# Kernel optimization log

Hardware: AMD Instinct MI355X
Metric: run time of the kernel (lower is better)

The kernel has to match this reference:

```python
import jax, jax.numpy as jnp
import numpy as np

B, T, C, H = 2, 2048, 1024, 16
D = C // H  # head dim = 64


def setup_inputs() -> dict:
    key = jax.random.key(0)
    ks = jax.random.split(key, 9)
    x = jax.random.normal(ks[0], (B, T, C), dtype=jnp.float32)
    # causal mask: True above the diagonal => positions to mask out
    mask = jnp.triu(jnp.ones((T, T), dtype=bool), k=1)[None, None]  # [1,1,T,T]
    s = 0.02
    Wq = jax.random.normal(ks[1], (C, C), dtype=jnp.float32) * s
    Wk = jax.random.normal(ks[2], (C, C), dtype=jnp.float32) * s
    Wv = jax.random.normal(ks[3], (C, C), dtype=jnp.float32) * s
    Wo = jax.random.normal(ks[4], (C, C), dtype=jnp.float32) * s
    bq = jax.random.normal(ks[5], (C,), dtype=jnp.float32) * s
    bk = jax.random.normal(ks[6], (C,), dtype=jnp.float32) * s
    bv = jax.random.normal(ks[7], (C,), dtype=jnp.float32) * s
    bo = jax.random.normal(ks[8], (C,), dtype=jnp.float32) * s
    return {"x": x, "mask": mask, "Wq": Wq, "bq": bq, "Wk": Wk, "bk": bk,
            "Wv": Wv, "bv": bv, "Wo": Wo, "bo": bo}


def reference(x, mask, Wq, bq, Wk, bk, Wv, bv, Wo, bo):
    b, t, c = x.shape
    # QKV projections, split heads -> [B,H,T,D]
    q = (x @ Wq + bq).reshape(b, t, H, D).transpose(0, 2, 1, 3)
    k = (x @ Wk + bk).reshape(b, t, H, D).transpose(0, 2, 1, 3)
    v = (x @ Wv + bv).reshape(b, t, H, D).transpose(0, 2, 1, 3)
    # scaled dot-product scores [B,H,T,T]
    att = jnp.einsum('bhtd,bhsd->bhts', q, k) * (1.0 / jnp.sqrt(jnp.float32(D)))
    att = jnp.where(mask, jnp.float32(-jnp.inf), att)
    att = jax.nn.softmax(att, axis=-1)  # dropout p=0.0 -> identity
    y = jnp.einsum('bhts,bhsd->bhtd', att, v)  # [B,H,T,D]
    y = y.transpose(0, 2, 1, 3).reshape(b, t, c)
    return y @ Wo + bo
```

## Files before the change

### kernel.cpp

```cpp
#include <hip/hip_runtime.h>
#include <hip/hip_bf16.h>

#define BB 2
#define TT 2048
#define CC 1024
#define HH 16
#define DD 64
#define MM (BB*TT)

typedef float f32x4 __attribute__((ext_vector_type(4)));
typedef __bf16 bf16x8 __attribute__((ext_vector_type(8)));
typedef unsigned int u32x4 __attribute__((ext_vector_type(4)));
typedef unsigned int u32x2 __attribute__((ext_vector_type(2)));

__device__ __forceinline__ unsigned short f2bf(float f) {
    unsigned int u = __float_as_uint(f);
    u += 0x7fff + ((u >> 16) & 1);
    return (unsigned short)(u >> 16);
}
__device__ __forceinline__ unsigned int pk2(float a, float b) {
    return (unsigned int)f2bf(a) | ((unsigned int)f2bf(b) << 16);
}

__device__ __forceinline__ void gload_lds16(const void* g, void* l) {
    __builtin_amdgcn_global_load_lds(
        (const __attribute__((address_space(1))) unsigned int*)(unsigned long long)g,
        (__attribute__((address_space(3))) unsigned int*)(unsigned int)(unsigned long long)l,
        16, 0, 0);
}

__global__ __launch_bounds__(256) void cvt_f32_bf16(
    const float* __restrict__ in, unsigned short* __restrict__ out)
{
    const size_t i = (size_t)blockIdx.x * 256 + threadIdx.x;
    const float4* in4 = (const float4*)in;
    float4 a = in4[2 * i], b = in4[2 * i + 1];
    u32x4 o;
    o[0] = pk2(a.x, a.y); o[1] = pk2(a.z, a.w);
    o[2] = pk2(b.x, b.y); o[3] = pk2(b.z, b.w);
    *(u32x4*)(out + 8 * i) = o;
}

__global__ __launch_bounds__(256) void wtrans_kernel(
    const float* __restrict__ W0, const float* __restrict__ W1,
    const float* __restrict__ W2, const float* __restrict__ W3,
    unsigned short* __restrict__ wt)
{
    const int tid = threadIdx.x;
    const int n0 = blockIdx.x * 64;
    const int k0 = blockIdx.y * 64;
    const int which = blockIdx.z;
    const float* W = (which == 0) ? W0 : (which == 1) ? W1 : (which == 2) ? W2 : W3;

    __shared__ float t_lds[64][68];

    #pragma unroll
    for (int p = 0; p < 4; ++p) {
        int idx = tid + p * 256;
        int r   = idx >> 4;
        int c4  = (idx & 15) * 4;
        *(float4*)&t_lds[r][c4] = *(const float4*)(W + (size_t)(k0 + r) * CC + n0 + c4);
    }
    __syncthreads();

    const int nl = tid >> 2;
    const int ks = (tid & 3) * 16;
    unsigned int w[8];
    #pragma unroll
    for (int j = 0; j < 8; ++j)
        w[j] = pk2(t_lds[ks + 2 * j][nl], t_lds[ks + 2 * j + 1][nl]);
    unsigned short* dst = wt + (size_t)which * CC * CC + (size_t)(n0 + nl) * CC + k0 + ks;
    u32x4 o0; o0[0] = w[0]; o0[1] = w[1]; o0[2] = w[2]; o0[3] = w[3];
    u32x4 o1; o1[0] = w[4]; o1[1] = w[5]; o1[2] = w[6]; o1[3] = w[7];
    *(u32x4*)dst = o0;
    *(u32x4*)(dst + 8) = o1;
}

__global__ __launch_bounds__(256) void gemm_qkv_mfma(
    const unsigned short* __restrict__ xbf, const unsigned short* __restrict__ wt,
    const float* __restrict__ bq, const float* __restrict__ bk, const float* __restrict__ bv,
    unsigned short* __restrict__ qbf, unsigned short* __restrict__ kbf,
    unsigned short* __restrict__ vtbf)
{
    const int tid = threadIdx.x;
    const int m0 = blockIdx.y * 128;
    const int nc0 = blockIdx.x * 128;
    const int which = nc0 >> 10;
    const int cb = nc0 & 1023;
    const unsigned short* Bt = wt + (size_t)which * CC * CC;
    const float* bias = (which == 0) ? bq : (which == 1) ? bk : bv;

    __shared__ __align__(16) unsigned short lds_a[128][32];
    __shared__ __align__(16) unsigned short lds_b[128][32];
    __shared__ __align__(16) unsigned short ebuf[128][136];

    const int lane = tid & 63;
    const int wv = tid >> 6;
    const int wm = (wv & 1) * 64;
    const int wn = (wv >> 1) * 64;
    const int fr = lane & 15;
    const int ks = lane >> 4;

    const int lrow = lane >> 2;
    const int lcol = (lane & 3) * 8;

    f32x4 acc[4][4];
    #pragma unroll
    for (int i = 0; i < 4; ++i)
        #pragma unroll
        for (int j = 0; j < 4; ++j) { acc[i][j][0]=0.f; acc[i][j][1]=0.f; acc[i][j][2]=0.f; acc[i][j][3]=0.f; }

    for (int k0 = 0; k0 < CC; k0 += 32) {
        __syncthreads();
        #pragma unroll
        for (int c = 0; c < 2; ++c) {
            const int r0 = (wv * 2 + c) * 16;
            gload_lds16(xbf + (size_t)(m0 + r0 + lrow) * CC + k0 + lcol, &lds_a[r0][0]);
            gload_lds16(Bt  + (size_t)(cb + r0 + lrow) * CC + k0 + lcol, &lds_b[r0][0]);
        }
        __syncthreads();

        bf16x8 af[4], bfv[4];
        #pragma unroll
        for (int i = 0; i < 4; ++i) {
            af[i]  = __builtin_bit_cast(bf16x8, *(const u32x4*)&lds_a[wm + i * 16 + fr][ks * 8]);
            bfv[i] = __builtin_bit_cast(bf16x8, *(const u32x4*)&lds_b[wn + i * 16 + fr][ks * 8]);
        }
        #pragma unroll
        for (int mi = 0; mi < 4; ++mi)
            #pragma unroll
            for (int ni = 0; ni < 4; ++ni)
                acc[mi][ni] = __builtin_amdgcn_mfma_f32_16x16x32_bf16(af[mi], bfv[ni], acc[mi][ni], 0, 0, 0);
    }

    if (which != 2) {
        const float scl = (which == 0) ? 0.125f : 1.0f;
        #pragma unroll
        for (int ni = 0; ni < 4; ++ni) {
            const int c_l = wn + ni * 16 + fr;
            const float bv2 = bias[cb + c_l];
            #pragma unroll
            for (int mi = 0; mi < 4; ++mi)
                #pragma unroll
                for (int j = 0; j < 4; ++j)
                    ebuf[wm + mi * 16 + ks * 4 + j][c_l] = f2bf((acc[mi][ni][j] + bv2) * scl);
        }
        __syncthreads();
        unsigned short* dst = (which == 0) ? qbf : kbf;
        #pragma unroll
        for (int p = 0; p < 8; ++p) {
            const int chunk = tid + p * 256;
            const int m_l = chunk >> 4;
            const int c_l8 = (chunk & 15) * 8;
            const int m = m0 + m_l;
            const int b = m >> 11, t = m & 2047;
            const int c = cb + c_l8;
            const int h = c >> 6, d = c & 63;
            *(u32x4*)(dst + (((size_t)(b * HH + h) * TT + t) * DD) + d) =
                *(const u32x4*)&ebuf[m_l][c_l8];
        }
    } else {
        #pragma unroll
        for (int ni = 0; ni < 4; ++ni) {
            const int c_l = wn + ni * 16 + fr;
            const float bv2 = bias[cb + c_l];
            #pragma unroll
            for (int mi = 0; mi < 4; ++mi) {
                const int m_l = wm + mi * 16 + ks * 4;
                unsigned int* q2 = (unsigned int*)&ebuf[c_l][m_l];
                q2[0] = pk2(acc[mi][ni][0] + bv2, acc[mi][ni][1] + bv2);
                q2[1] = pk2(acc[mi][ni][2] + bv2, acc[mi][ni][3] + bv2);
            }
        }
        __syncthreads();
        #pragma unroll
        for (int p = 0; p < 8; ++p) {
            const int chunk = tid + p * 256;
            const int c_l = chunk >> 4;
            const int t_l8 = (chunk & 15) * 8;
            const int c = cb + c_l;
            const int h = c >> 6, d = c & 63;
            const int b = m0 >> 11, t = (m0 & 2047) + t_l8;
            *(u32x4*)(vtbf + ((size_t)(b * HH + h) * DD + d) * TT + t) =
                *(const u32x4*)&ebuf[c_l][t_l8];
        }
    }
}

__global__ __launch_bounds__(256) void attn_mfma(
    const unsigned short* __restrict__ qbf, const unsigned short* __restrict__ kbf,
    const unsigned short* __restrict__ vtbf, unsigned short* __restrict__ ybf)
{
    const int tid  = threadIdx.x;
    const int w    = tid >> 6;
    const int lane = tid & 63;
    const int g    = lane >> 4;
    const int i    = lane & 15;
    const int qi   = 31 - (int)blockIdx.x;
    const int h    = blockIdx.y;
    const int bb   = blockIdx.z;
    const int q0   = qi * 64;
    const size_t hq = (size_t)(bb * HH + h) * TT * DD;
    const size_t hv = (size_t)(bb * HH + h) * DD * TT;

    __shared__ __align__(16) unsigned short k_lds[64][64];
    __shared__ __align__(16) unsigned short vt_lds[64][64];
    __shared__ __align__(16) unsigned short p_lds[64][64];

    bf16x8 qf[2];
    {
        const unsigned short* qrow = qbf + hq + (size_t)(q0 + 16 * w + i) * DD + g * 8;
        qf[0] = __builtin_bit_cast(bf16x8, *(const u32x4*)qrow);
        qf[1] = __builtin_bit_cast(bf16x8, *(const u32x4*)(qrow + 32));
    }

    f32x4 oT[4];
    #pragma unroll
    for (int ni = 0; ni < 4; ++ni) { oT[ni][0]=0.f; oT[ni][1]=0.f; oT[ni][2]=0.f; oT[ni][3]=0.f; }
    float m_i = -1e30f, l_i = 0.0f;

    const int srow  = tid >> 3;
    const int sc    = tid & 7;
    const int swoff = ((sc ^ (srow & 7)) << 3);

    const int i7 = i & 7;

    const int nt = qi + 1;
    u32x4 kreg0 = *(const u32x4*)(kbf + hq + (size_t)srow * DD + sc * 8);
    u32x4 kreg1 = *(const u32x4*)(kbf + hq + (size_t)(srow + 32) * DD + sc * 8);
    u32x4 vreg0 = *(const u32x4*)(vtbf + hv + (size_t)srow * TT + sc * 8);
    u32x4 vreg1 = *(const u32x4*)(vtbf + hv + (size_t)(srow + 32) * TT + sc * 8);

    for (int kk = 0; kk < nt; ++kk) {
        __syncthreads();
        *(u32x4*)&k_lds[srow][swoff]       = kreg0;
        *(u32x4*)&k_lds[srow + 32][swoff]  = kreg1;
        *(u32x4*)&vt_lds[srow][swoff]      = vreg0;
        *(u32x4*)&vt_lds[srow + 32][swoff] = vreg1;
        __syncthreads();
        if (kk + 1 < nt) {
            const int s1 = (kk + 1) * 64;
            kreg0 = *(const u32x4*)(kbf + hq + (size_t)(s1 + srow) * DD + sc * 8);
            kreg1 = *(const u32x4*)(kbf + hq + (size_t)(s1 + srow + 32) * DD + sc * 8);
            vreg0 = *(const u32x4*)(vtbf + hv + (size_t)srow * TT + s1 + sc * 8);
            vreg1 = *(const u32x4*)(vtbf + hv + (size_t)(srow + 32) * TT + s1 + sc * 8);
        }

        f32x4 sT[4];
        #pragma unroll
        for (int ni = 0; ni < 4; ++ni) { sT[ni][0]=0.f; sT[ni][1]=0.f; sT[ni][2]=0.f; sT[ni][3]=0.f; }
        #pragma unroll
        for (int lks = 0; lks < 2; ++lks)
            #pragma unroll
            for (int ni = 0; ni < 4; ++ni) {
                bf16x8 ka = __builtin_bit_cast(bf16x8,
                    *(const u32x4*)&k_lds[ni * 16 + i][((lks * 4 + g) ^ i7) << 3]);
                sT[ni] = __builtin_amdgcn_mfma_f32_16x16x32_bf16(ka, qf[lks], sT[ni], 0, 0, 0);
            }

        if (kk == qi) {
            const int q_l = 16 * w + i;
            #pragma unroll
            for (int ni = 0; ni < 4; ++ni)
                #pragma unroll
                for (int reg = 0; reg < 4; ++reg)
                    if (ni * 16 + 4 * g + reg > q_l) sT[ni][reg] = -1e30f;
        }

        float tmax = sT[0][0];
        #pragma unroll
        for (int ni = 0; ni < 4; ++ni)
            #pragma unroll
            for (int e = 0; e < 4; ++e) tmax = fmaxf(tmax, sT[ni][e]);
        tmax = fmaxf(tmax, __shfl_xor(tmax, 16));
        tmax = fmaxf(tmax, __shfl_xor(tmax, 32));
        const float m_new = fmaxf(m_i, tmax);
        const float alpha = __expf(m_i - m_new);
        float lsum = 0.f;
        #pragma unroll
        for (int ni = 0; ni < 4; ++ni)
            #pragma unroll
            for (int e = 0; e < 4; ++e) {
                float pv = __expf(sT[ni][e] - m_new);
                sT[ni][e] = pv;
                lsum += pv;
            }
        lsum += __shfl_xor(lsum, 16);
        lsum += __shfl_xor(lsum, 32);
        l_i = l_i * alpha + lsum;
        m_i = m_new;
        #pragma unroll
        for (int ni = 0; ni < 4; ++ni)
            #pragma unroll
            for (int e = 0; e < 4; ++e) oT[ni][e] *= alpha;

        #pragma unroll
        for (int ni = 0; ni < 4; ++ni) {
            u32x2 pr;
            pr[0] = pk2(sT[ni][0], sT[ni][1]);
            pr[1] = pk2(sT[ni][2], sT[ni][3]);
            const int pcol = (((2 * ni + (g >> 1)) ^ i7) << 3) | (4 * (g & 1));
            *(u32x2*)&p_lds[16 * w + i][pcol] = pr;
        }

        #pragma unroll
        for (int lks = 0; lks < 2; ++lks) {
            bf16x8 pb = __builtin_bit_cast(bf16x8,
                *(const u32x4*)&p_lds[16 * w + i][((lks * 4 + g) ^ i7) << 3]);
            #pragma unroll
            for (int ni = 0; ni < 4; ++ni) {
                bf16x8 va = __builtin_bit_cast(bf16x8,
                    *(const u32x4*)&vt_lds[ni * 16 + i][((lks * 4 + g) ^ i7) << 3]);
                oT[ni] = __builtin_amdgcn_mfma_f32_16x16x32_bf16(va, pb, oT[ni], 0, 0, 0);
            }
        }
    }

    const float inv = 1.0f / l_i;
    unsigned short* ybase = ybf + ((size_t)bb * TT + (q0 + 16 * w + i)) * CC + h * DD;
    #pragma unroll
    for (int ni = 0; ni < 4; ++ni) {
        u32x2 st;
        st[0] = pk2(oT[ni][0] * inv, oT[ni][1] * inv);
        st[1] = pk2(oT[ni][2] * inv, oT[ni][3] * inv);
        *(u32x2*)(ybase + ni * 16 + 4 * g) = st;
    }
}

__global__ __launch_bounds__(256) void gemm_out_mfma(
    const unsigned short* __restrict__ ybf, const unsigned short* __restrict__ wt_o,
    const float* __restrict__ bo, float* __restrict__ out)
{
    const int tid = threadIdx.x;
    const int m0 = blockIdx.y * 128;
    const int n0 = blockIdx.x * 128;

    __shared__ __align__(16) unsigned short lds_a[128][32];
    __shared__ __align__(16) unsigned short lds_b[128][32];

    const int lane = tid & 63;
    const int wv = tid >> 6;
    const int wm = (wv & 1) * 64;
    const int wn = (wv >> 1) * 64;
    const int fr = lane & 15;
    const int ks = lane >> 4;
    const int lrow = lane >> 2;
    const int lcol = (lane & 3) * 8;

    f32x4 acc[4][4];
    #pragma unroll
    for (int i = 0; i < 4; ++i)
        #pragma unroll
        for (int j = 0; j < 4; ++j) { acc[i][j][0]=0.f; acc[i][j][1]=0.f; acc[i][j][2]=0.f; acc[i][j][3]=0.f; }

    for (int k0 = 0; k0 < CC; k0 += 32) {
        __syncthreads();
        #pragma unroll
        for (int c = 0; c < 2; ++c) {
            const int r0 = (wv * 2 + c) * 16;
            gload_lds16(ybf  + (size_t)(m0 + r0 + lrow) * CC + k0 + lcol, &lds_a[r0][0]);
            gload_lds16(wt_o + (size_t)(n0 + r0 + lrow) * CC + k0 + lcol, &lds_b[r0][0]);
        }
        __syncthreads();

        bf16x8 af[4], bfv[4];
        #pragma unroll
        for (int i = 0; i < 4; ++i) {
            af[i]  = __builtin_bit_cast(bf16x8, *(const u32x4*)&lds_a[wm + i * 16 + fr][ks * 8]);
            bfv[i] = __builtin_bit_cast(bf16x8, *(const u32x4*)&lds_b[wn + i * 16 + fr][ks * 8]);
        }
        #pragma unroll
        for (int mi = 0; mi < 4; ++mi)
            #pragma unroll
            for (int ni = 0; ni < 4; ++ni)
                acc[mi][ni] = __builtin_amdgcn_mfma_f32_16x16x32_bf16(af[mi], bfv[ni], acc[mi][ni], 0, 0, 0);
    }

    #pragma unroll
    for (int ni = 0; ni < 4; ++ni) {
        const int n = n0 + wn + ni * 16 + fr;
        const float bv2 = bo[n];
        #pragma unroll
        for (int mi = 0; mi < 4; ++mi) {
            #pragma unroll
            for (int j = 0; j < 4; ++j) {
                const int m = m0 + wm + mi * 16 + ks * 4 + j;
                out[(size_t)m * CC + n] = acc[mi][ni][j] + bv2;
            }
        }
    }
}

extern "C" void kernel_launch(void* const* d_in, const int* in_sizes, int n_in,
                              void* d_out, int out_size, void* d_ws, size_t ws_size,
                              hipStream_t stream) {
    const float* x  = (const float*)d_in[0];
    const float* Wq = (const float*)d_in[2];
    const float* bq = (const float*)d_in[3];
    const float* Wk = (const float*)d_in[4];
    const float* bk = (const float*)d_in[5];
    const float* Wv = (const float*)d_in[6];
    const float* bv = (const float*)d_in[7];
    const float* Wo = (const float*)d_in[8];
    const float* bo = (const float*)d_in[9];
    float* out = (float*)d_out;

    const size_t NE = (size_t)MM * CC;
    unsigned short* xbf  = (unsigned short*)d_ws;
    unsigned short* ybf  = xbf + NE;
    unsigned short* wt   = ybf + NE;
    unsigned short* qbf  = wt + (size_t)4 * CC * CC;
    unsigned short* kbf  = qbf + NE;
    unsigned short* vtbf = kbf + NE;

    cvt_f32_bf16<<<2048, 256, 0, stream>>>(x, xbf);
    wtrans_kernel<<<dim3(16, 16, 4), 256, 0, stream>>>(Wq, Wk, Wv, Wo, wt);
    gemm_qkv_mfma<<<dim3(24, 32), 256, 0, stream>>>(
        xbf, wt, bq, bk, bv, qbf, kbf, vtbf);
    attn_mfma<<<dim3(TT / 64, HH, BB), 256, 0, stream>>>(qbf, kbf, vtbf, ybf);
    gemm_out_mfma<<<dim3(8, 32), 256, 0, stream>>>(
        ybf, wt + (size_t)3 * CC * CC, bo, out);
}
```

Baseline: 249.0 us.

## Double attention KV tile to 128 keys with per-wave causal MFMA skipping

The flash-attention kernel now processes 128 keys per iteration instead of 64, halving the number of loop iterations and block-wide barriers per query tile. K/V staging, register prefetch, P buffer and swizzles are widened to the 128-key tile. QK^T MFMAs are skipped for 16-key sub-blocks that lie entirely above a wave's causal diagonal. The larger tile raises LDS use and register pressure (8 score fragments, 8 prefetch registers), and the last tile may carry more masked work for odd query tiles.

```diff
diff --git a/kernel.cpp b/kernel.cpp
--- a/kernel.cpp
+++ b/kernel.cpp
@@ -203,9 +203,9 @@
     const size_t hq = (size_t)(bb * HH + h) * TT * DD;
     const size_t hv = (size_t)(bb * HH + h) * DD * TT;
 
-    __shared__ __align__(16) unsigned short k_lds[64][64];
-    __shared__ __align__(16) unsigned short vt_lds[64][64];
-    __shared__ __align__(16) unsigned short p_lds[64][64];
+    __shared__ __align__(16) unsigned short k_lds[128][64];
+    __shared__ __align__(16) unsigned short vt_lds[64][128];
+    __shared__ __align__(16) unsigned short p_lds[64][128];
 
     bf16x8 qf[2];
     {
@@ -219,57 +219,69 @@
     for (int ni = 0; ni < 4; ++ni) { oT[ni][0]=0.f; oT[ni][1]=0.f; oT[ni][2]=0.f; oT[ni][3]=0.f; }
     float m_i = -1e30f, l_i = 0.0f;
 
-    const int srow  = tid >> 3;
-    const int sc    = tid & 7;
-    const int swoff = ((sc ^ (srow & 7)) << 3);
+    const int skrow = tid >> 3;
+    const int skc   = tid & 7;
+    const int skoff = ((skc ^ (skrow & 7)) << 3);
+    const int svrow = tid >> 4;
+    const int svc   = tid & 15;
+    const int svoff = (((svc & 8) | ((svc & 7) ^ (svrow & 7))) << 3);
 
     const int i7 = i & 7;
 
-    const int nt = qi + 1;
-    u32x4 kreg0 = *(const u32x4*)(kbf + hq + (size_t)srow * DD + sc * 8);
-    u32x4 kreg1 = *(const u32x4*)(kbf + hq + (size_t)(srow + 32) * DD + sc * 8);
-    u32x4 vreg0 = *(const u32x4*)(vtbf + hv + (size_t)srow * TT + sc * 8);
-    u32x4 vreg1 = *(const u32x4*)(vtbf + hv + (size_t)(srow + 32) * TT + sc * 8);
+    const int nt = (qi >> 1) + 1;
+    u32x4 kreg[4], vreg[4];
+    #pragma unroll
+    for (int p = 0; p < 4; ++p)
+        kreg[p] = *(const u32x4*)(kbf + hq + (size_t)(skrow + 32 * p) * DD + skc * 8);
+    #pragma unroll
+    for (int p = 0; p < 4; ++p)
+        vreg[p] = *(const u32x4*)(vtbf + hv + (size_t)(svrow + 16 * p) * TT + svc * 8);
 
     for (int kk = 0; kk < nt; ++kk) {
-        __syncthreads();
-        *(u32x4*)&k_lds[srow][swoff]       = kreg0;
-        *(u32x4*)&k_lds[srow + 32][swoff]  = kreg1;
-        *(u32x4*)&vt_lds[srow][swoff]      = vreg0;
-        *(u32x4*)&vt_lds[srow + 32][swoff] = vreg1;
+        const int s0 = kk * 128;
+        __syncthreads();
+        #pragma unroll
+        for (int p = 0; p < 4; ++p) *(u32x4*)&k_lds[skrow + 32 * p][skoff] = kreg[p];
+        #pragma unroll
+        for (int p = 0; p < 4; ++p) *(u32x4*)&vt_lds[svrow + 16 * p][svoff] = vreg[p];
         __syncthreads();
         if (kk + 1 < nt) {
-            const int s1 = (kk + 1) * 64;
-            kreg0 = *(const u32x4*)(kbf + hq + (size_t)(s1 + srow) * DD + sc * 8);
-            kreg1 = *(const u32x4*)(kbf + hq + (size_t)(s1 + srow + 32) * DD + sc * 8);
-            vreg0 = *(const u32x4*)(vtbf + hv + (size_t)srow * TT + s1 + sc * 8);
-            vreg1 = *(const u32x4*)(vtbf + hv + (size_t)(srow + 32) * TT + s1 + sc * 8);
-        }
-
-        f32x4 sT[4];
-        #pragma unroll
-        for (int ni = 0; ni < 4; ++ni) { sT[ni][0]=0.f; sT[ni][1]=0.f; sT[ni][2]=0.f; sT[ni][3]=0.f; }
-        #pragma unroll
-        for (int lks = 0; lks < 2; ++lks)
-            #pragma unroll
-            for (int ni = 0; ni < 4; ++ni) {
-                bf16x8 ka = __builtin_bit_cast(bf16x8,
-                    *(const u32x4*)&k_lds[ni * 16 + i][((lks * 4 + g) ^ i7) << 3]);
-                sT[ni] = __builtin_amdgcn_mfma_f32_16x16x32_bf16(ka, qf[lks], sT[ni], 0, 0, 0);
+            const int s1 = (kk + 1) * 128;
+            #pragma unroll
+            for (int p = 0; p < 4; ++p)
+                kreg[p] = *(const u32x4*)(kbf + hq + (size_t)(s1 + skrow + 32 * p) * DD + skc * 8);
+            #pragma unroll
+            for (int p = 0; p < 4; ++p)
+                vreg[p] = *(const u32x4*)(vtbf + hv + (size_t)(svrow + 16 * p) * TT + s1 + svc * 8);
+        }
+
+        f32x4 sT[8];
+        #pragma unroll
+        for (int ni = 0; ni < 8; ++ni) { sT[ni][0]=0.f; sT[ni][1]=0.f; sT[ni][2]=0.f; sT[ni][3]=0.f; }
+        #pragma unroll
+        for (int ni = 0; ni < 8; ++ni) {
+            if (s0 + ni * 16 <= q0 + 16 * w + 15) {
+                #pragma unroll
+                for (int lks = 0; lks < 2; ++lks) {
+                    bf16x8 ka = __builtin_bit_cast(bf16x8,
+                        *(const u32x4*)&k_lds[ni * 16 + i][((lks * 4 + g) ^ i7) << 3]);
+                    sT[ni] = __builtin_amdgcn_mfma_f32_16x16x32_bf16(ka, qf[lks], sT[ni], 0, 0, 0);
+                }
             }
-
-        if (kk == qi) {
-            const int q_l = 16 * w + i;
-            #pragma unroll
-            for (int ni = 0; ni < 4; ++ni)
+        }
+
+        if (kk == nt - 1) {
+            const int q_glob = q0 + 16 * w + i;
+            #pragma unroll
+            for (int ni = 0; ni < 8; ++ni)
                 #pragma unroll
                 for (int reg = 0; reg < 4; ++reg)
-                    if (ni * 16 + 4 * g + reg > q_l) sT[ni][reg] = -1e30f;
+                    if (s0 + ni * 16 + 4 * g + reg > q_glob) sT[ni][reg] = -1e30f;
         }
 
         float tmax = sT[0][0];
         #pragma unroll
-        for (int ni = 0; ni < 4; ++ni)
+        for (int ni = 0; ni < 8; ++ni)
             #pragma unroll
             for (int e = 0; e < 4; ++e) tmax = fmaxf(tmax, sT[ni][e]);
         tmax = fmaxf(tmax, __shfl_xor(tmax, 16));
@@ -278,7 +290,7 @@
         const float alpha = __expf(m_i - m_new);
         float lsum = 0.f;
         #pragma unroll
-        for (int ni = 0; ni < 4; ++ni)
+        for (int ni = 0; ni < 8; ++ni)
             #pragma unroll
             for (int e = 0; e < 4; ++e) {
                 float pv = __expf(sT[ni][e] - m_new);
@@ -295,22 +307,25 @@
             for (int e = 0; e < 4; ++e) oT[ni][e] *= alpha;
 
         #pragma unroll
-        for (int ni = 0; ni < 4; ++ni) {
+        for (int ni = 0; ni < 8; ++ni) {
             u32x2 pr;
             pr[0] = pk2(sT[ni][0], sT[ni][1]);
             pr[1] = pk2(sT[ni][2], sT[ni][3]);
-            const int pcol = (((2 * ni + (g >> 1)) ^ i7) << 3) | (4 * (g & 1));
+            const int ch = 2 * ni + (g >> 1);
+            const int pcol = (((ch & 8) | ((ch & 7) ^ i7)) << 3) | (4 * (g & 1));
             *(u32x2*)&p_lds[16 * w + i][pcol] = pr;
         }
 
         #pragma unroll
-        for (int lks = 0; lks < 2; ++lks) {
+        for (int lks = 0; lks < 4; ++lks) {
+            const int c = lks * 4 + g;
+            const int coff = (((c & 8) | ((c & 7) ^ i7)) << 3);
             bf16x8 pb = __builtin_bit_cast(bf16x8,
-                *(const u32x4*)&p_lds[16 * w + i][((lks * 4 + g) ^ i7) << 3]);
+                *(const u32x4*)&p_lds[16 * w + i][coff]);
             #pragma unroll
             for (int ni = 0; ni < 4; ++ni) {
                 bf16x8 va = __builtin_bit_cast(bf16x8,
-                    *(const u32x4*)&vt_lds[ni * 16 + i][((lks * 4 + g) ^ i7) << 3]);
+                    *(const u32x4*)&vt_lds[ni * 16 + i][coff]);
                 oT[ni] = __builtin_amdgcn_mfma_f32_16x16x32_bf16(va, pb, oT[ni], 0, 0, 0);
             }
         }
```

Measured after the change: 382.0 us. 1.53x slower.
